# Kernel tuning notes

Hardware: AMD Instinct MI355X
Metric: run time of the kernel (lower is better)

## Reference

```python
import jax, jax.numpy as jnp
from jax import lax
import numpy as np

NUM_CH, LSTM_SIZE, NUM_CLS, SEQ_LEN, NUM_PROPS = 128, 512, 40, 256, 1024

def setup_inputs() -> dict:
    key = jax.random.key(0)
    ks = jax.random.split(key, 16)
    s = 0.05
    H, C = LSTM_SIZE, NUM_CH
    return {
        "data": jax.random.normal(ks[0], (NUM_PROPS, SEQ_LEN, C), jnp.float32),
        "labels": jax.random.randint(ks[1], (NUM_PROPS, 2), 0, NUM_CLS).astype(jnp.int32),
        "proposals": jax.random.uniform(ks[2], (NUM_PROPS, 2), jnp.float32),
        # layer 0 LSTM params (PyTorch gate order i,f,g,o; b = b_ih + b_hh)
        "W_ih_0": jax.random.normal(ks[3], (4 * H, C), jnp.float32) * s,
        "W_hh_0": jax.random.normal(ks[4], (4 * H, H), jnp.float32) * s,
        "b_0": jax.random.normal(ks[5], (4 * H,), jnp.float32) * s,
        # layer 1 LSTM params
        "W_ih_1": jax.random.normal(ks[6], (4 * H, H), jnp.float32) * s,
        "W_hh_1": jax.random.normal(ks[7], (4 * H, H), jnp.float32) * s,
        "b_1": jax.random.normal(ks[8], (4 * H,), jnp.float32) * s,
        # heads
        "W_cls": jax.random.normal(ks[9], (NUM_CLS, H), jnp.float32) * s,
        "b_cls": jnp.zeros((NUM_CLS,), jnp.float32),
        "W_bbox": jax.random.normal(ks[10], (2, H), jnp.float32) * s,
        "b_bbox": jnp.zeros((2,), jnp.float32),
    }

def _lstm_layer(x_tnc, W_ih, W_hh, b):
    # x_tnc: [T, N, C_in]; returns hidden sequence [T, N, H]
    T, N, _ = x_tnc.shape
    H = W_hh.shape[1]
    xg = jnp.einsum('tnc,gc->tng', x_tnc, W_ih) + b  # precompute input projections
    def step(carry, gx):
        h, c = carry
        g = gx + h @ W_hh.T
        i, f, gg, o = jnp.split(g, 4, axis=-1)
        i, f, o = jax.nn.sigmoid(i), jax.nn.sigmoid(f), jax.nn.sigmoid(o)
        c = f * c + i * jnp.tanh(gg)
        h = o * jnp.tanh(c)
        return (h, c), h
    h0 = jnp.zeros((N, H), x_tnc.dtype)
    _, hs = lax.scan(step, (h0, h0), xg)
    return hs

def _forward(data, labels, proposals,
             W_ih_0, W_hh_0, b_0, W_ih_1, W_hh_1, b_1,
             W_cls, b_cls, W_bbox, b_bbox):
    x = jnp.transpose(data, (1, 0, 2))  # [T, N, C]
    x = _lstm_layer(x, W_ih_0, W_hh_0, b_0)
    hs = _lstm_layer(x, W_ih_1, W_hh_1, b_1)
    base_feat = hs[-1]                   # last timestep, [N, H]
    cls_feat = base_feat @ W_cls.T + b_cls
    bbox_feat = base_feat @ W_bbox.T + b_bbox
    # train branch: cross-entropy / loss_div, smooth_l1 * 10
    lbl = labels[:, 0]
    logp = jax.nn.log_softmax(cls_feat, axis=-1)
    cls_loss = -jnp.mean(jnp.take_along_axis(logp, lbl[:, None], axis=1))
    cls_idx = jnp.argmax(cls_feat, axis=1)
    loss_div = 1.0 + jnp.sum((cls_idx == lbl).astype(cls_feat.dtype))
    cls_loss = cls_loss / lax.stop_gradient(loss_div)
    target = proposals / SEQ_LEN
    diff = jnp.abs(bbox_feat - target)
    sl1 = jnp.where(diff < 1.0, 0.5 * diff * diff, diff - 0.5)
    bbox_loss = jnp.mean(sl1) * 10.0
    return jnp.stack([cls_loss, bbox_loss])

def reference(data, labels, proposals,
              W_ih_0, W_hh_0, b_0, W_ih_1, W_hh_1, b_1,
              W_cls, b_cls, W_bbox, b_bbox):
    return _forward(data, labels, proposals,
                    W_ih_0, W_hh_0, b_0, W_ih_1, W_hh_1, b_1,
                    W_cls, b_cls, W_bbox, b_bbox)
```

## Files before the change

kernel.cpp:

```cpp
#include <hip/hip_runtime.h>

typedef unsigned short u16;
typedef __attribute__((ext_vector_type(8))) __bf16 bf16x8;
typedef __attribute__((ext_vector_type(4))) float f32x4;

#define T_SEQ 256
#define N_B   1024
#define C_IN  128
#define H_DIM 512
#define NCLS  40
#define NT0   20
#define NT1   32
#define HSLOT (16*1024*32)

union B8 { bf16x8 v; u16 s[8]; };

__device__ __forceinline__ u16 f32_to_bf16_rne(float x) {
    unsigned u = __float_as_uint(x);
    unsigned rounding = 0x7FFFu + ((u >> 16) & 1u);
    return (u16)((u + rounding) >> 16);
}
__device__ __forceinline__ float bf16_to_f32(u16 h) {
    return __uint_as_float(((unsigned)h) << 16);
}
__device__ __forceinline__ void split2(float x, u16& hi, u16& lo) {
    u16 h = f32_to_bf16_rne(x);
    float hf = bf16_to_f32(h);
    u16 l = f32_to_bf16_rne(x - hf);
    hi = h; lo = l;
}
__device__ __forceinline__ float fast_sigmoid(float x) {
    return 1.0f / (1.0f + __expf(-x));
}
__device__ __forceinline__ float fast_tanh(float x) {
    return 1.0f - 2.0f / (__expf(2.0f * x) + 1.0f);
}

__global__ void k_pack_w(const float* __restrict__ Wih, const float* __restrict__ Whh,
                         int KX, int NT, u16* __restrict__ hi, u16* __restrict__ lo) {
    size_t idx = (size_t)blockIdx.x * 256 + threadIdx.x;
    size_t total = (size_t)16 * NT * 128 * 32;
    if (idx >= total) return;
    int k = (int)(idx & 31);
    int r = (int)((idx >> 5) & 127);
    int rem = (int)(idx >> 12);
    int kt = rem % NT, ct = rem / NT;
    int gate = r & 3, jl = r >> 2;
    int srow = (gate << 9) + (ct << 5) + jl;
    int kg = (kt << 5) + k;
    float v = (kg < KX) ? Wih[(size_t)srow * KX + kg] : Whh[(size_t)srow * H_DIM + (kg - KX)];
    u16 h, l; split2(v, h, l);
    hi[idx] = h; lo[idx] = l;
}

__device__ __forceinline__ void lstm_tile_body(
    int local_blk,
    const float* __restrict__ Xf32,
    const u16* __restrict__ xAhi, const u16* __restrict__ xAlo, int nxt,
    const u16* __restrict__ hAhi, const u16* __restrict__ hAlo,
    const u16* __restrict__ Whi, const u16* __restrict__ Wlo, int NT,
    const float* __restrict__ bias, float* __restrict__ cbuf,
    u16* __restrict__ oHhi, u16* __restrict__ oHlo, float* __restrict__ oF32,
    char* lds, float* biasT)
{
    int ct = ((blockIdx.x & 7) << 1) | ((local_blk >> 6) & 1);
    int rt = (local_blk >> 3) & 7;
    int n0 = rt << 7;

    int tid  = threadIdx.x;
    int w    = tid >> 6;
    int l    = tid & 63;
    int quad = l >> 4;
    int lr   = l & 15;
    int grp  = w >> 2;
    int wr   = (w & 1) << 6;
    int wc2  = ((w >> 1) & 1) << 6;

    if (tid < 128)
        biasT[tid] = bias[((tid & 3) << 9) + (ct << 5) + (tid >> 2)];

    const size_t wbase = ((size_t)(ct * NT)) << 12;
    bf16x8 sa_h[2], sa_l[2], sb_h[2], sb_l[2];

    auto load_stage = [&](int ss) {
        #pragma unroll
        for (int g = 0; g < 2; g++) {
            int kt = (ss << 1) | g;
            size_t wo = wbase + ((size_t)kt << 12) + ((size_t)tid << 3);
            sb_h[g] = *(const bf16x8*)(Whi + wo);
            sb_l[g] = *(const bf16x8*)(Wlo + wo);
            if (Xf32 != nullptr && kt < nxt) {
                int row = tid >> 2, seg = tid & 3;
                const float* p = Xf32 + (size_t)(n0 + row) * 32768 + (kt << 5) + (seg << 3);
                f32x4 x0 = *(const f32x4*)p;
                f32x4 x1 = *(const f32x4*)(p + 4);
                B8 hh, ll;
                #pragma unroll
                for (int e = 0; e < 4; e++) { u16 a, b; split2(x0[e], a, b); hh.s[e] = a; ll.s[e] = b; }
                #pragma unroll
                for (int e = 0; e < 4; e++) { u16 a, b; split2(x1[e], a, b); hh.s[4 + e] = a; ll.s[4 + e] = b; }
                sa_h[g] = hh.v; sa_l[g] = ll.v;
            } else {
                const u16 *ph, *pl; int kk;
                if (kt < nxt) { ph = xAhi; pl = xAlo; kk = kt; }
                else          { ph = hAhi; pl = hAlo; kk = kt - nxt; }
                size_t ao = (((size_t)kk * 1024 + n0) << 5) + ((size_t)tid << 3);
                sa_h[g] = *(const bf16x8*)(ph + ao);
                sa_l[g] = *(const bf16x8*)(pl + ao);
            }
        }
    };
    auto write_stage = [&](char* buf) {
        #pragma unroll
        for (int g = 0; g < 2; g++) {
            char* p = buf + (g << 13) + (tid << 4);
            *(bf16x8*)(p)          = sa_h[g];
            *(bf16x8*)(p + 16384)  = sa_l[g];
            *(bf16x8*)(p + 32768)  = sb_h[g];
            *(bf16x8*)(p + 49152)  = sb_l[g];
        }
    };

    f32x4 acc[4][4];
    #pragma unroll
    for (int i = 0; i < 4; i++)
        #pragma unroll
        for (int j = 0; j < 4; j++)
            acc[i][j] = (f32x4){0.f, 0.f, 0.f, 0.f};

    const int NS = NT >> 1;
    load_stage(0);
    write_stage(lds);
    __syncthreads();

    for (int ss = 0; ss < NS; ss++) {
        char* cur = lds + ((ss & 1) << 16) + (grp << 13);
        if (ss + 1 < NS) load_stage(ss + 1);

        bf16x8 ah[4], al[4];
        #pragma unroll
        for (int i = 0; i < 4; i++) {
            int ro = ((wr + (i << 4) + lr) << 6) + (quad << 4);
            ah[i] = *(const bf16x8*)(cur + ro);
            al[i] = *(const bf16x8*)(cur + 16384 + ro);
        }
        #pragma unroll
        for (int jp = 0; jp < 2; jp++) {
            bf16x8 bh[2], bl[2];
            #pragma unroll
            for (int u = 0; u < 2; u++) {
                int j = (jp << 1) | u;
                int ro = ((wc2 + (j << 4) + lr) << 6) + (quad << 4);
                bh[u] = *(const bf16x8*)(cur + 32768 + ro);
                bl[u] = *(const bf16x8*)(cur + 49152 + ro);
            }
            __builtin_amdgcn_s_setprio(1);
            #pragma unroll
            for (int u = 0; u < 2; u++) {
                int j = (jp << 1) | u;
                #pragma unroll
                for (int i = 0; i < 4; i++) {
                    acc[i][j] = __builtin_amdgcn_mfma_f32_16x16x32_bf16(ah[i], bh[u], acc[i][j], 0, 0, 0);
                    acc[i][j] = __builtin_amdgcn_mfma_f32_16x16x32_bf16(al[i], bh[u], acc[i][j], 0, 0, 0);
                    acc[i][j] = __builtin_amdgcn_mfma_f32_16x16x32_bf16(ah[i], bl[u], acc[i][j], 0, 0, 0);
                }
            }
            __builtin_amdgcn_s_setprio(0);
        }

        if (ss + 1 < NS) write_stage(lds + (((ss + 1) & 1) << 16));
        __syncthreads();
    }

    float* G0 = (float*)lds;
    float* G1 = (float*)(lds + 65536);
    {
        float* myG = grp ? G1 : G0;
        #pragma unroll
        for (int i = 0; i < 4; i++)
            #pragma unroll
            for (int j = 0; j < 4; j++)
                #pragma unroll
                for (int r = 0; r < 4; r++)
                    myG[(wr + (i << 4) + (quad << 2) + r) * 128 + wc2 + (j << 4) + lr] = acc[i][j][r];
    }
    __syncthreads();

    int jl = tid & 31;
    int rbase = tid >> 5;
    #pragma unroll
    for (int it = 0; it < 8; it++) {
        int row = rbase + (it << 4);
        f32x4 g0 = *(const f32x4*)(G0 + row * 128 + (jl << 2));
        f32x4 g1 = *(const f32x4*)(G1 + row * 128 + (jl << 2));
        float gi = g0[0] + g1[0] + biasT[(jl << 2) + 0];
        float gf = g0[1] + g1[1] + biasT[(jl << 2) + 1];
        float gg = g0[2] + g1[2] + biasT[(jl << 2) + 2];
        float go = g0[3] + g1[3] + biasT[(jl << 2) + 3];
        float si = fast_sigmoid(gi);
        float sf = fast_sigmoid(gf);
        float so = fast_sigmoid(go);
        int n = n0 + row;
        int cidx = (n << 9) + (ct << 5) + jl;
        float cn = sf * cbuf[cidx] + si * fast_tanh(gg);
        cbuf[cidx] = cn;
        float h = so * fast_tanh(cn);
        u16 hh2, hl2; split2(h, hh2, hl2);
        size_t ho = (((size_t)ct * 1024 + n) << 5) + jl;
        oHhi[ho] = hh2; oHlo[ho] = hl2;
        if (oF32) oF32[cidx] = h;
    }
}

__global__ __launch_bounds__(512) void k_lstm_pair(
    int t, const float* __restrict__ data,
    const u16* __restrict__ W0hi, const u16* __restrict__ W0lo,
    const u16* __restrict__ W1hi, const u16* __restrict__ W1lo,
    const float* __restrict__ b0, const float* __restrict__ b1,
    u16* __restrict__ h0hi, u16* __restrict__ h0lo,
    u16* __restrict__ h1hi, u16* __restrict__ h1lo,
    float* __restrict__ c0, float* __restrict__ c1,
    float* __restrict__ bfeat)
{
    __shared__ __align__(16) char lds[131072];
    __shared__ float biasT[128];
    int local_blk = blockIdx.x & 127;

    if (blockIdx.x < 128) {
        if (t == 0) return;
        int s = t - 1;
        const u16* xh = h0hi + (size_t)(s & 1) * HSLOT;
        const u16* xl = h0lo + (size_t)(s & 1) * HSLOT;
        const u16* hh = h1hi + (size_t)((s - 1) & 1) * HSLOT;
        const u16* hl = h1lo + (size_t)((s - 1) & 1) * HSLOT;
        u16* oh = h1hi + (size_t)(s & 1) * HSLOT;
        u16* ol = h1lo + (size_t)(s & 1) * HSLOT;
        lstm_tile_body(local_blk, nullptr, xh, xl, 16, hh, hl,
                       W1hi, W1lo, NT1, b1, c1, oh, ol,
                       (s == T_SEQ - 1) ? bfeat : nullptr, lds, biasT);
    } else {
        if (t >= T_SEQ) return;
        const u16* hh = h0hi + (size_t)((t - 1) & 1) * HSLOT;
        const u16* hl = h0lo + (size_t)((t - 1) & 1) * HSLOT;
        u16* oh = h0hi + (size_t)(t & 1) * HSLOT;
        u16* ol = h0lo + (size_t)(t & 1) * HSLOT;
        lstm_tile_body(local_blk, data + (size_t)t * C_IN, nullptr, nullptr, 4,
                       hh, hl, W0hi, W0lo, NT0, b0, c0, oh, ol,
                       nullptr, lds, biasT);
    }
}

__global__ __launch_bounds__(64) void k_head(
    const float* __restrict__ hfeat, const float* __restrict__ Wcls, const float* __restrict__ bcls,
    const float* __restrict__ Wbb, const float* __restrict__ bbb,
    const int* __restrict__ labels, const float* __restrict__ props,
    float* __restrict__ accum)
{
    __shared__ float hs[H_DIM];
    __shared__ float logits[NCLS];
    __shared__ float bb[2];
    int n = blockIdx.x, t = threadIdx.x;
    for (int k = t; k < H_DIM; k += 64) hs[k] = hfeat[((size_t)n << 9) + k];
    __syncthreads();
    if (t < NCLS) {
        float s = bcls[t];
        const float* w = Wcls + (size_t)t * H_DIM;
        for (int k = 0; k < H_DIM; k++) s += hs[k] * w[k];
        logits[t] = s;
    } else if (t < NCLS + 2) {
        int j = t - NCLS;
        float s = bbb[j];
        const float* w = Wbb + (size_t)j * H_DIM;
        for (int k = 0; k < H_DIM; k++) s += hs[k] * w[k];
        bb[j] = s;
    }
    __syncthreads();
    if (t == 0) {
        float m = logits[0]; int am = 0;
        for (int j = 1; j < NCLS; j++) if (logits[j] > m) { m = logits[j]; am = j; }
        float se = 0.f;
        for (int j = 0; j < NCLS; j++) se += expf(logits[j] - m);
        int lbl = labels[n * 2];
        float logp = logits[lbl] - m - logf(se);
        atomicAdd(&accum[0], -logp);
        if (am == lbl) atomicAdd(&accum[1], 1.0f);
        float s2 = 0.f;
        for (int j = 0; j < 2; j++) {
            float target = props[n * 2 + j] * (1.0f / 256.0f);
            float d = fabsf(bb[j] - target);
            s2 += (d < 1.f) ? 0.5f * d * d : d - 0.5f;
        }
        atomicAdd(&accum[2], s2);
    }
}

__global__ void k_final(const float* __restrict__ accum, float* __restrict__ out) {
    out[0] = (accum[0] * (1.0f / 1024.0f)) / (1.0f + accum[1]);
    out[1] = accum[2] * (10.0f / 2048.0f);
}

extern "C" void kernel_launch(void* const* d_in, const int* in_sizes, int n_in,
                              void* d_out, int out_size, void* d_ws, size_t ws_size,
                              hipStream_t stream) {
    const float* data  = (const float*)d_in[0];
    const int*   labels= (const int*)d_in[1];
    const float* props = (const float*)d_in[2];
    const float* Wih0  = (const float*)d_in[3];
    const float* Whh0  = (const float*)d_in[4];
    const float* b0    = (const float*)d_in[5];
    const float* Wih1  = (const float*)d_in[6];
    const float* Whh1  = (const float*)d_in[7];
    const float* b1    = (const float*)d_in[8];
    const float* Wcls  = (const float*)d_in[9];
    const float* bcls  = (const float*)d_in[10];
    const float* Wbb   = (const float*)d_in[11];
    const float* bbb   = (const float*)d_in[12];
    float* out = (float*)d_out;

    char* ws = (char*)d_ws;
    size_t off = 0;
    auto alloc = [&](size_t bytes) -> void* {
        void* p = ws + off;
        off = (off + bytes + 255) & ~(size_t)255;
        return p;
    };
    const size_t NH = (size_t)N_B * H_DIM;
    const size_t W0E = (size_t)16 * NT0 * 128 * 32;
    const size_t W1E = (size_t)16 * NT1 * 128 * 32;

    u16* W0hi = (u16*)alloc(W0E * 2);
    u16* W0lo = (u16*)alloc(W0E * 2);
    u16* W1hi = (u16*)alloc(W1E * 2);
    u16* W1lo = (u16*)alloc(W1E * 2);
    u16* h0hi = (u16*)alloc(2 * (size_t)HSLOT * 2);
    u16* h0lo = (u16*)alloc(2 * (size_t)HSLOT * 2);
    u16* h1hi = (u16*)alloc(2 * (size_t)HSLOT * 2);
    u16* h1lo = (u16*)alloc(2 * (size_t)HSLOT * 2);
    float* c0   = (float*)alloc(NH * 4);
    float* c1   = (float*)alloc(NH * 4);
    float* bfeat= (float*)alloc(NH * 4);
    float* accum= (float*)alloc(4 * 4);

    k_pack_w<<<(int)(W0E / 256), 256, 0, stream>>>(Wih0, Whh0, C_IN, NT0, W0hi, W0lo);
    k_pack_w<<<(int)(W1E / 256), 256, 0, stream>>>(Wih1, Whh1, H_DIM, NT1, W1hi, W1lo);

    (void)hipMemsetAsync(h0hi + HSLOT, 0, (size_t)HSLOT * 2, stream);
    (void)hipMemsetAsync(h0lo + HSLOT, 0, (size_t)HSLOT * 2, stream);
    (void)hipMemsetAsync(h1hi + HSLOT, 0, (size_t)HSLOT * 2, stream);
    (void)hipMemsetAsync(h1lo + HSLOT, 0, (size_t)HSLOT * 2, stream);
    (void)hipMemsetAsync(c0, 0, NH * 4, stream);
    (void)hipMemsetAsync(c1, 0, NH * 4, stream);
    (void)hipMemsetAsync(accum, 0, 16, stream);

    for (int t = 0; t <= T_SEQ; t++) {
        k_lstm_pair<<<256, 512, 0, stream>>>(
            t, data, W0hi, W0lo, W1hi, W1lo, b0, b1,
            h0hi, h0lo, h1hi, h1lo, c0, c1, bfeat);
    }

    k_head<<<N_B, 64, 0, stream>>>(bfeat, Wcls, bcls, Wbb, bbb, labels, props, accum);
    k_final<<<1, 1, 0, stream>>>(accum, out);
}
```

Before: 7.984 ms.

## Replace per-timestep launches with a persistent cooperative kernel and grid sync

Replaces the 257 per-timestep kernel launches with one cooperative persistent kernel that loops over time and uses grid.sync between steps. The LSTM cell state now lives in registers instead of global c buffers, and the bias is loaded into LDS once rather than every step. This removes launch overhead and the cell-state global traffic per step, at the cost of a grid-wide barrier each step and a residency requirement of 256 blocks of 512 threads with about 128KB of LDS each. The launch bounds hint of two blocks per CU may raise register pressure.

```diff
diff --git a/kernel.cpp b/kernel.cpp
--- a/kernel.cpp
+++ b/kernel.cpp
@@ -1,4 +1,7 @@
 #include <hip/hip_runtime.h>
+#include <hip/hip_cooperative_groups.h>
+
+namespace cg = cooperative_groups;
 
 typedef unsigned short u16;
 typedef __attribute__((ext_vector_type(8))) __bf16 bf16x8;
@@ -54,19 +57,15 @@
 }
 
 __device__ __forceinline__ void lstm_tile_body(
-    int local_blk,
+    int ct, int n0,
     const float* __restrict__ Xf32,
     const u16* __restrict__ xAhi, const u16* __restrict__ xAlo, int nxt,
     const u16* __restrict__ hAhi, const u16* __restrict__ hAlo,
     const u16* __restrict__ Whi, const u16* __restrict__ Wlo, int NT,
-    const float* __restrict__ bias, float* __restrict__ cbuf,
+    float* __restrict__ creg,
     u16* __restrict__ oHhi, u16* __restrict__ oHlo, float* __restrict__ oF32,
-    char* lds, float* biasT)
+    char* lds, const float* biasT)
 {
-    int ct = ((blockIdx.x & 7) << 1) | ((local_blk >> 6) & 1);
-    int rt = (local_blk >> 3) & 7;
-    int n0 = rt << 7;
-
     int tid  = threadIdx.x;
     int w    = tid >> 6;
     int l    = tid & 63;
@@ -75,9 +74,6 @@
     int grp  = w >> 2;
     int wr   = (w & 1) << 6;
     int wc2  = ((w >> 1) & 1) << 6;
-
-    if (tid < 128)
-        biasT[tid] = bias[((tid & 3) << 9) + (ct << 5) + (tid >> 2)];
 
     const size_t wbase = ((size_t)(ct * NT)) << 12;
     bf16x8 sa_h[2], sa_l[2], sb_h[2], sb_l[2];
@@ -201,52 +197,70 @@
         float sf = fast_sigmoid(gf);
         float so = fast_sigmoid(go);
         int n = n0 + row;
-        int cidx = (n << 9) + (ct << 5) + jl;
-        float cn = sf * cbuf[cidx] + si * fast_tanh(gg);
-        cbuf[cidx] = cn;
+        float cn = sf * creg[it] + si * fast_tanh(gg);
+        creg[it] = cn;
         float h = so * fast_tanh(cn);
         u16 hh2, hl2; split2(h, hh2, hl2);
         size_t ho = (((size_t)ct * 1024 + n) << 5) + jl;
         oHhi[ho] = hh2; oHlo[ho] = hl2;
-        if (oF32) oF32[cidx] = h;
-    }
-}
-
-__global__ __launch_bounds__(512) void k_lstm_pair(
-    int t, const float* __restrict__ data,
+        if (oF32) oF32[((size_t)n << 9) + (ct << 5) + jl] = h;
+    }
+}
+
+__global__ __launch_bounds__(512, 2) void k_lstm_persist(
+    const float* __restrict__ data,
     const u16* __restrict__ W0hi, const u16* __restrict__ W0lo,
     const u16* __restrict__ W1hi, const u16* __restrict__ W1lo,
     const float* __restrict__ b0, const float* __restrict__ b1,
     u16* __restrict__ h0hi, u16* __restrict__ h0lo,
     u16* __restrict__ h1hi, u16* __restrict__ h1lo,
-    float* __restrict__ c0, float* __restrict__ c1,
     float* __restrict__ bfeat)
 {
+    cg::grid_group grid = cg::this_grid();
     __shared__ __align__(16) char lds[131072];
     __shared__ float biasT[128];
+
     int local_blk = blockIdx.x & 127;
-
-    if (blockIdx.x < 128) {
-        if (t == 0) return;
-        int s = t - 1;
-        const u16* xh = h0hi + (size_t)(s & 1) * HSLOT;
-        const u16* xl = h0lo + (size_t)(s & 1) * HSLOT;
-        const u16* hh = h1hi + (size_t)((s - 1) & 1) * HSLOT;
-        const u16* hl = h1lo + (size_t)((s - 1) & 1) * HSLOT;
-        u16* oh = h1hi + (size_t)(s & 1) * HSLOT;
-        u16* ol = h1lo + (size_t)(s & 1) * HSLOT;
-        lstm_tile_body(local_blk, nullptr, xh, xl, 16, hh, hl,
-                       W1hi, W1lo, NT1, b1, c1, oh, ol,
-                       (s == T_SEQ - 1) ? bfeat : nullptr, lds, biasT);
-    } else {
-        if (t >= T_SEQ) return;
-        const u16* hh = h0hi + (size_t)((t - 1) & 1) * HSLOT;
-        const u16* hl = h0lo + (size_t)((t - 1) & 1) * HSLOT;
-        u16* oh = h0hi + (size_t)(t & 1) * HSLOT;
-        u16* ol = h0lo + (size_t)(t & 1) * HSLOT;
-        lstm_tile_body(local_blk, data + (size_t)t * C_IN, nullptr, nullptr, 4,
-                       hh, hl, W0hi, W0lo, NT0, b0, c0, oh, ol,
-                       nullptr, lds, biasT);
+    bool isL1 = blockIdx.x < 128;
+    int ct = ((blockIdx.x & 7) << 1) | ((local_blk >> 6) & 1);
+    int n0 = ((local_blk >> 3) & 7) << 7;
+
+    const float* bias = isL1 ? b1 : b0;
+    if (threadIdx.x < 128)
+        biasT[threadIdx.x] = bias[((threadIdx.x & 3) << 9) + (ct << 5) + (threadIdx.x >> 2)];
+    __syncthreads();
+
+    float creg[8];
+    #pragma unroll
+    for (int i = 0; i < 8; i++) creg[i] = 0.f;
+
+    for (int t = 0; t <= T_SEQ; t++) {
+        if (isL1) {
+            if (t > 0) {
+                int s = t - 1;
+                const u16* xh = h0hi + (size_t)(s & 1) * HSLOT;
+                const u16* xl = h0lo + (size_t)(s & 1) * HSLOT;
+                const u16* hh = h1hi + (size_t)((s - 1) & 1) * HSLOT;
+                const u16* hl = h1lo + (size_t)((s - 1) & 1) * HSLOT;
+                u16* oh = h1hi + (size_t)(s & 1) * HSLOT;
+                u16* ol = h1lo + (size_t)(s & 1) * HSLOT;
+                lstm_tile_body(ct, n0, nullptr, xh, xl, 16, hh, hl,
+                               W1hi, W1lo, NT1, creg, oh, ol,
+                               (s == T_SEQ - 1) ? bfeat : nullptr, lds, biasT);
+            }
+        } else {
+            if (t < T_SEQ) {
+                const u16* hh = h0hi + (size_t)((t - 1) & 1) * HSLOT;
+                const u16* hl = h0lo + (size_t)((t - 1) & 1) * HSLOT;
+                u16* oh = h0hi + (size_t)(t & 1) * HSLOT;
+                u16* ol = h0lo + (size_t)(t & 1) * HSLOT;
+                lstm_tile_body(ct, n0, data + (size_t)t * C_IN, nullptr, nullptr, 4,
+                               hh, hl, W0hi, W0lo, NT0, creg, oh, ol,
+                               nullptr, lds, biasT);
+            }
+        }
+        __threadfence();
+        grid.sync();
     }
 }
 
@@ -336,8 +350,6 @@
     u16* h0lo = (u16*)alloc(2 * (size_t)HSLOT * 2);
     u16* h1hi = (u16*)alloc(2 * (size_t)HSLOT * 2);
     u16* h1lo = (u16*)alloc(2 * (size_t)HSLOT * 2);
-    float* c0   = (float*)alloc(NH * 4);
-    float* c1   = (float*)alloc(NH * 4);
     float* bfeat= (float*)alloc(NH * 4);
     float* accum= (float*)alloc(4 * 4);
 
@@ -348,14 +360,27 @@
     (void)hipMemsetAsync(h0lo + HSLOT, 0, (size_t)HSLOT * 2, stream);
     (void)hipMemsetAsync(h1hi + HSLOT, 0, (size_t)HSLOT * 2, stream);
     (void)hipMemsetAsync(h1lo + HSLOT, 0, (size_t)HSLOT * 2, stream);
-    (void)hipMemsetAsync(c0, 0, NH * 4, stream);
-    (void)hipMemsetAsync(c1, 0, NH * 4, stream);
     (void)hipMemsetAsync(accum, 0, 16, stream);
 
-    for (int t = 0; t <= T_SEQ; t++) {
-        k_lstm_pair<<<256, 512, 0, stream>>>(
-            t, data, W0hi, W0lo, W1hi, W1lo, b0, b1,
-            h0hi, h0lo, h1hi, h1lo, c0, c1, bfeat);
+    {
+        const float* a_data = data;
+        const u16* a_W0hi = W0hi; const u16* a_W0lo = W0lo;
+        const u16* a_W1hi = W1hi; const u16* a_W1lo = W1lo;
+        const float* a_b0 = b0;   const float* a_b1 = b1;
+        u16* a_h0hi = h0hi; u16* a_h0lo = h0lo;
+        u16* a_h1hi = h1hi; u16* a_h1lo = h1lo;
+        float* a_bfeat = bfeat;
+        void* kargs[] = {
+            (void*)&a_data,
+            (void*)&a_W0hi, (void*)&a_W0lo,
+            (void*)&a_W1hi, (void*)&a_W1lo,
+            (void*)&a_b0, (void*)&a_b1,
+            (void*)&a_h0hi, (void*)&a_h0lo,
+            (void*)&a_h1hi, (void*)&a_h1lo,
+            (void*)&a_bfeat
+        };
+        (void)hipLaunchCooperativeKernel((const void*)k_lstm_persist,
+                                         dim3(256), dim3(512), kargs, 0, stream);
     }
 
     k_head<<<N_B, 64, 0, stream>>>(bfeat, Wcls, bcls, Wbb, bbb, labels, props, accum);
```

After: 27.02 ms. 238% more time.

## Use direct global-to-LDS loads for weight/hidden tiles and swizzle gate scratch

Applied to the files above, without the earlier changes.

Replaces the register-staged prefetch of the packed bf16 weight and activation tiles with global_load_lds so they land in LDS without passing through VGPRs. Only the fp32 input path, which needs hi/lo splitting, still goes through registers. It also XOR-swizzles the column index of the fp32 gate scratch to reduce LDS bank conflicts in the epilogue. This lowers register pressure and removes VALU store work, but it depends on the async LDS writes being ordered correctly by the existing barriers and on the per-wave 1KB layout matching the previous per-thread layout.

```diff
diff --git a/kernel.cpp b/kernel.cpp
--- a/kernel.cpp
+++ b/kernel.cpp
@@ -34,6 +34,13 @@
 }
 __device__ __forceinline__ float fast_tanh(float x) {
     return 1.0f - 2.0f / (__expf(2.0f * x) + 1.0f);
+}
+
+__device__ __forceinline__ void glds16(const void* g, void* l) {
+    __builtin_amdgcn_global_load_lds(
+        (const __attribute__((address_space(1))) void*)(unsigned long long)(g),
+        (__attribute__((address_space(3))) void*)(unsigned int)(unsigned long long)(l),
+        16, 0, 0);
 }
 
 __global__ void k_pack_w(const float* __restrict__ Wih, const float* __restrict__ Whh,
@@ -80,44 +87,48 @@
         biasT[tid] = bias[((tid & 3) << 9) + (ct << 5) + (tid >> 2)];
 
     const size_t wbase = ((size_t)(ct * NT)) << 12;
-    bf16x8 sa_h[2], sa_l[2], sb_h[2], sb_l[2];
-
-    auto load_stage = [&](int ss) {
+    bf16x8 sxh[2], sxl[2];
+
+    auto stage_ss = [&](int ss, char* buf) {
         #pragma unroll
         for (int g = 0; g < 2; g++) {
             int kt = (ss << 1) | g;
+            char* wavebase = buf + (g << 13) + ((tid >> 6) << 10);
             size_t wo = wbase + ((size_t)kt << 12) + ((size_t)tid << 3);
-            sb_h[g] = *(const bf16x8*)(Whi + wo);
-            sb_l[g] = *(const bf16x8*)(Wlo + wo);
-            if (Xf32 != nullptr && kt < nxt) {
-                int row = tid >> 2, seg = tid & 3;
-                const float* p = Xf32 + (size_t)(n0 + row) * 32768 + (kt << 5) + (seg << 3);
-                f32x4 x0 = *(const f32x4*)p;
-                f32x4 x1 = *(const f32x4*)(p + 4);
-                B8 hh, ll;
-                #pragma unroll
-                for (int e = 0; e < 4; e++) { u16 a, b; split2(x0[e], a, b); hh.s[e] = a; ll.s[e] = b; }
-                #pragma unroll
-                for (int e = 0; e < 4; e++) { u16 a, b; split2(x1[e], a, b); hh.s[4 + e] = a; ll.s[4 + e] = b; }
-                sa_h[g] = hh.v; sa_l[g] = ll.v;
-            } else {
+            glds16(Whi + wo, wavebase + 32768);
+            glds16(Wlo + wo, wavebase + 49152);
+            if (Xf32 == nullptr || kt >= nxt) {
                 const u16 *ph, *pl; int kk;
                 if (kt < nxt) { ph = xAhi; pl = xAlo; kk = kt; }
                 else          { ph = hAhi; pl = hAlo; kk = kt - nxt; }
                 size_t ao = (((size_t)kk * 1024 + n0) << 5) + ((size_t)tid << 3);
-                sa_h[g] = *(const bf16x8*)(ph + ao);
-                sa_l[g] = *(const bf16x8*)(pl + ao);
+                glds16(ph + ao, wavebase);
+                glds16(pl + ao, wavebase + 16384);
             }
         }
     };
-    auto write_stage = [&](char* buf) {
+    auto loadX = [&](int ss) {
+        #pragma unroll
+        for (int g = 0; g < 2; g++) {
+            int kt = (ss << 1) | g;
+            int row = tid >> 2, seg = tid & 3;
+            const float* p = Xf32 + (size_t)(n0 + row) * 32768 + (kt << 5) + (seg << 3);
+            f32x4 x0 = *(const f32x4*)p;
+            f32x4 x1 = *(const f32x4*)(p + 4);
+            B8 hh, ll;
+            #pragma unroll
+            for (int e = 0; e < 4; e++) { u16 a, b; split2(x0[e], a, b); hh.s[e] = a; ll.s[e] = b; }
+            #pragma unroll
+            for (int e = 0; e < 4; e++) { u16 a, b; split2(x1[e], a, b); hh.s[4 + e] = a; ll.s[4 + e] = b; }
+            sxh[g] = hh.v; sxl[g] = ll.v;
+        }
+    };
+    auto writeX = [&](char* buf) {
         #pragma unroll
         for (int g = 0; g < 2; g++) {
             char* p = buf + (g << 13) + (tid << 4);
-            *(bf16x8*)(p)          = sa_h[g];
-            *(bf16x8*)(p + 16384)  = sa_l[g];
-            *(bf16x8*)(p + 32768)  = sb_h[g];
-            *(bf16x8*)(p + 49152)  = sb_l[g];
+            *(bf16x8*)(p)         = sxh[g];
+            *(bf16x8*)(p + 16384) = sxl[g];
         }
     };
 
@@ -129,13 +140,18 @@
             acc[i][j] = (f32x4){0.f, 0.f, 0.f, 0.f};
 
     const int NS = NT >> 1;
-    load_stage(0);
-    write_stage(lds);
+    stage_ss(0, lds);
+    if (Xf32 != nullptr) { loadX(0); writeX(lds); }
     __syncthreads();
 
     for (int ss = 0; ss < NS; ss++) {
-        char* cur = lds + ((ss & 1) << 16) + (grp << 13);
-        if (ss + 1 < NS) load_stage(ss + 1);
+        char* buf  = lds + ((ss & 1) << 16);
+        char* cur  = buf + (grp << 13);
+        char* nbuf = lds + (((ss + 1) & 1) << 16);
+        bool pf  = (ss + 1 < NS);
+        bool pfX = pf && (Xf32 != nullptr) && (((ss + 1) << 1) < nxt);
+        if (pf) stage_ss(ss + 1, nbuf);
+        if (pfX) loadX(ss + 1);
 
         bf16x8 ah[4], al[4];
         #pragma unroll
@@ -168,7 +184,7 @@
             __builtin_amdgcn_s_setprio(0);
         }
 
-        if (ss + 1 < NS) write_stage(lds + (((ss + 1) & 1) << 16));
+        if (pfX) writeX(nbuf);
         __syncthreads();
     }
 
@@ -181,8 +197,11 @@
             #pragma unroll
             for (int j = 0; j < 4; j++)
                 #pragma unroll
-                for (int r = 0; r < 4; r++)
-                    myG[(wr + (i << 4) + (quad << 2) + r) * 128 + wc2 + (j << 4) + lr] = acc[i][j][r];
+                for (int r = 0; r < 4; r++) {
+                    int rr = wr + (i << 4) + (quad << 2) + r;
+                    int col = wc2 + (j << 4) + lr;
+                    myG[rr * 128 + (col ^ (((rr >> 2) & 3) << 2))] = acc[i][j][r];
+                }
     }
     __syncthreads();
 
@@ -191,8 +210,9 @@
     #pragma unroll
     for (int it = 0; it < 8; it++) {
         int row = rbase + (it << 4);
-        f32x4 g0 = *(const f32x4*)(G0 + row * 128 + (jl << 2));
-        f32x4 g1 = *(const f32x4*)(G1 + row * 128 + (jl << 2));
+        int cS = (jl << 2) ^ (((row >> 2) & 3) << 2);
+        f32x4 g0 = *(const f32x4*)(G0 + row * 128 + cS);
+        f32x4 g1 = *(const f32x4*)(G1 + row * 128 + cS);
         float gi = g0[0] + g1[0] + biasT[(jl << 2) + 0];
         float gf = g0[1] + g1[1] + biasT[(jl << 2) + 1];
         float gg = g0[2] + g1[2] + biasT[(jl << 2) + 2];
```

After: 7.188 ms. -10.0%, faster.
